# Kernel optimization log

Measured on AMD Instinct MI355X. Metric: run time of the kernel, lower is better.

Reference implementation:

```python
import jax, jax.numpy as jnp
import numpy as np

N_NODES = 50000
N_EDGES = 800000
IN_DIM = 128
EMB = 128
EDGE_DIM = 16
N_LAYERS = 4
BATCH = 64


def setup_inputs() -> dict:
    key = jax.random.key(0)
    ks = jax.random.split(key, 12)
    x = jax.random.normal(ks[0], (N_NODES, IN_DIM), dtype=jnp.float32)
    edge_index = jax.random.randint(ks[1], (2, N_EDGES), 0, N_NODES, dtype=jnp.int64)
    edge_attr = jax.random.normal(ks[2], (N_EDGES, EDGE_DIM), dtype=jnp.float32)
    batch = jnp.sort(jax.random.randint(ks[3], (N_NODES,), 0, BATCH, dtype=jnp.int64))

    def glorot(k, shape):
        fan_in = shape[-2]
        return jax.random.normal(k, shape, dtype=jnp.float32) / jnp.sqrt(jnp.float32(fan_in))

    msg_in = 2 * EMB + EDGE_DIM  # [h_src, h_dst, edge_attr]
    upd_in = 2 * EMB             # [h, aggregated_messages]
    return {
        "x": x,
        "edge_index": edge_index,
        "edge_attr": edge_attr,
        "batch": batch,
        "W_in": glorot(ks[4], (IN_DIM, EMB)),
        "b_in": jnp.zeros((EMB,), jnp.float32),
        "W_msg": glorot(ks[5], (N_LAYERS, msg_in, EMB)),
        "b_msg": jnp.zeros((N_LAYERS, EMB), jnp.float32),
        "W_upd": glorot(ks[6], (N_LAYERS, upd_in, EMB)),
        "b_upd": jnp.zeros((N_LAYERS, EMB), jnp.float32),
        "W_pred": glorot(ks[7], (EMB, 1)),
        "b_pred": jnp.zeros((1,), jnp.float32),
    }


def reference(x, edge_index, edge_attr, batch,
              W_in, b_in, W_msg, b_msg, W_upd, b_upd, W_pred, b_pred):
    n_nodes = x.shape[0]
    src, dst = edge_index[0], edge_index[1]

    # lin_in
    h = x @ W_in + b_in  # [N, EMB]

    # stacked message-passing layers with residual adds
    for l in range(W_msg.shape[0]):  # small fixed layer loop
        # per-edge message: relu(Linear([h_src, h_dst, e]))
        m_in = jnp.concatenate([h[src], h[dst], edge_attr], axis=-1)  # [E, 2*EMB+ED]
        m = jax.nn.relu(m_in @ W_msg[l] + b_msg[l])                    # [E, EMB]
        # sum-aggregate messages at destination nodes
        agg = jax.ops.segment_sum(m, dst, num_segments=n_nodes)       # [N, EMB]
        # node update: relu(Linear([h, agg])); residual add (h = h + conv(h))
        u_in = jnp.concatenate([h, agg], axis=-1)                      # [N, 2*EMB]
        h = h + jax.nn.relu(u_in @ W_upd[l] + b_upd[l])

    # global mean pool over graphs in the batch
    counts = jax.ops.segment_sum(jnp.ones((n_nodes,), h.dtype), batch, num_segments=BATCH)
    h_graph = jax.ops.segment_sum(h, batch, num_segments=BATCH) / jnp.maximum(counts, 1.0)[:, None]

    # lin_pred + view(-1)
    out = h_graph @ W_pred + b_pred  # [BATCH, 1]
    return out.reshape(-1)
```

## Files before the change

### kernel.cpp

```cpp
#include <hip/hip_runtime.h>


#define THREADS 256

typedef __attribute__((ext_vector_type(8))) short short8v;
typedef __attribute__((ext_vector_type(4))) float f32x4;
typedef __attribute__((ext_vector_type(2))) float f32x2;

__device__ inline unsigned short f2bf(float f)
{
    unsigned int u = __float_as_uint(f);
    return (unsigned short)((u + 0x7FFFu + ((u >> 16) & 1u)) >> 16);
}

__device__ inline unsigned int cvt_pk_bf16(float lo, float hi)
{
    unsigned int r;
    asm("v_cvt_pk_bf16_f32 %0, %1, %2" : "=v"(r) : "v"(lo), "v"(hi));
    return r;
}

__global__ __launch_bounds__(THREADS)
void wconv_all(const float* __restrict__ W_in, const float* __restrict__ W_msg,
               const float* __restrict__ W_upd, unsigned short* __restrict__ wbf)
{
    int b = blockIdx.x;
    int job, kb;
    if (b < 576) { job = b >> 6; kb = b & 63; }
    else         { int r = b - 576; job = 9 + (r >> 7); kb = r & 127; }

    const float* src;
    unsigned short* dst;
    int K;
    if (job == 0)      { src = W_in;                                  dst = wbf;                               K = 128; }
    else if (job <= 4) { int l = job - 1; src = W_msg + (size_t)l * 272 * 128;             dst = wbf + 16384 + l * 32768;           K = 128; }
    else if (job <= 8) { int l = job - 5; src = W_msg + (size_t)l * 272 * 128 + 128 * 128; dst = wbf + 16384 + l * 32768 + 16384;   K = 128; }
    else               { int l = job - 9; src = W_upd + (size_t)l * 256 * 128;             dst = wbf + 147456 + l * 32768;          K = 256; }

    int i = kb * 256 + threadIdx.x;
    int k = i >> 7, n = i & 127;
    dst[n * K + k] = f2bf(src[i]);
}

__global__ __launch_bounds__(THREADS)
void f32_to_bf16(const float* __restrict__ in, unsigned short* __restrict__ out, int n4)
{
    int i = blockIdx.x * blockDim.x + threadIdx.x;
    int stride = gridDim.x * blockDim.x;
    for (; i < n4; i += stride) {
        float4 v = reinterpret_cast<const float4*>(in)[i];
        unsigned int lo = f2bf(v.x) | ((unsigned int)f2bf(v.y) << 16);
        unsigned int hi = f2bf(v.z) | ((unsigned int)f2bf(v.w) << 16);
        reinterpret_cast<uint2*>(out)[i] = make_uint2(lo, hi);
    }
}

template<int K, int CPW, bool FUSED2, bool RELU, bool RESID, bool WF32>
__global__ __launch_bounds__(THREADS)
void gemm_regW(const unsigned short* __restrict__ X1, const unsigned short* __restrict__ X2,
               const unsigned short* __restrict__ Wt, const float* __restrict__ bias,
               const float* __restrict__ resid, float* __restrict__ Cf,
               unsigned short* __restrict__ CbfA, unsigned short* __restrict__ CbfB,
               int M, int nTiles)
{
    constexpr int KS  = K / 32;
    constexpr int NC  = CPW * 64;
    constexpr int LST = NC + 4;
    __shared__ float Cls[32 * LST];

    const int t = threadIdx.x;
    const int w = t >> 6;
    const int l = t & 63;
    const int r  = l & 15;
    const int kb = l >> 4;
    const int wc = w * (CPW * 16);

    short8v b[CPW][KS];
#pragma unroll
    for (int c = 0; c < CPW; c++)
#pragma unroll
        for (int ks = 0; ks < KS; ks++)
            b[c][ks] = *reinterpret_cast<const short8v*>(
                Wt + (size_t)(wc + c * 16 + r) * K + ks * 32 + kb * 8);

    const int rrow = t >> 3;
    const int cb   = (t & 7) * (NC / 8);

    for (int tile = blockIdx.x; tile < nTiles; tile += gridDim.x) {
        const int mBase = tile * 32;
        const int row0 = min(mBase + r,      M - 1);
        const int row1 = min(mBase + 16 + r, M - 1);

        f32x4 acc[2][CPW];
#pragma unroll
        for (int mi = 0; mi < 2; mi++)
#pragma unroll
            for (int c = 0; c < CPW; c++) acc[mi][c] = (f32x4){0.f, 0.f, 0.f, 0.f};

#pragma unroll
        for (int ks = 0; ks < KS; ks++) {
            const unsigned short* Xs = X1;
            int ko = ks * 32;
            if (K == 256 && ko >= 128) { Xs = X2; ko -= 128; }
            const short8v a0 = *reinterpret_cast<const short8v*>(Xs + (size_t)row0 * 128 + ko + kb * 8);
            const short8v a1 = *reinterpret_cast<const short8v*>(Xs + (size_t)row1 * 128 + ko + kb * 8);
#pragma unroll
            for (int c = 0; c < CPW; c++) {
                acc[0][c] = __builtin_amdgcn_mfma_f32_16x16x32_bf16(a0, b[c][ks], acc[0][c], 0, 0, 0);
                acc[1][c] = __builtin_amdgcn_mfma_f32_16x16x32_bf16(a1, b[c][ks], acc[1][c], 0, 0, 0);
            }
        }

#pragma unroll
        for (int mi = 0; mi < 2; mi++)
#pragma unroll
            for (int c = 0; c < CPW; c++) {
                const int gc = wc + c * 16 + r;
#pragma unroll
                for (int j = 0; j < 4; j++)
                    Cls[(mi * 16 + kb * 4 + j) * LST + gc] = acc[mi][c][j];
            }
        __syncthreads();

        const int gr = mBase + rrow;
        if (gr < M) {
#pragma unroll
            for (int q = 0; q < NC / 64; q += 1) {
                f32x4 v0 = *reinterpret_cast<const f32x4*>(&Cls[rrow * LST + cb + q * 8]);
                f32x4 v1 = *reinterpret_cast<const f32x4*>(&Cls[rrow * LST + cb + q * 8 + 4]);
                const int col = cb + q * 8;

                if (FUSED2) {
                    if (col >= 128) {
                        v0 += *reinterpret_cast<const f32x4*>(bias + col - 128);
                        v1 += *reinterpret_cast<const f32x4*>(bias + col - 128 + 4);
                    }
                } else if (bias) {
                    v0 += *reinterpret_cast<const f32x4*>(bias + col);
                    v1 += *reinterpret_cast<const f32x4*>(bias + col + 4);
                }
                if (RELU) {
#pragma unroll
                    for (int i = 0; i < 4; i++) { v0[i] = fmaxf(v0[i], 0.f); v1[i] = fmaxf(v1[i], 0.f); }
                }
                if (RESID) {
                    v0 += *reinterpret_cast<const f32x4*>(resid + (size_t)gr * 128 + col);
                    v1 += *reinterpret_cast<const f32x4*>(resid + (size_t)gr * 128 + col + 4);
                }
                if (WF32) {
                    *reinterpret_cast<f32x4*>(Cf + (size_t)gr * 128 + col)     = v0;
                    *reinterpret_cast<f32x4*>(Cf + (size_t)gr * 128 + col + 4) = v1;
                }
                uint4 pk;
                pk.x = cvt_pk_bf16(v0[0], v0[1]);
                pk.y = cvt_pk_bf16(v0[2], v0[3]);
                pk.z = cvt_pk_bf16(v1[0], v1[1]);
                pk.w = cvt_pk_bf16(v1[2], v1[3]);
                if (FUSED2) {
                    if (col < 128)
                        *reinterpret_cast<uint4*>(CbfA + (size_t)gr * 128 + col) = pk;
                    else
                        *reinterpret_cast<uint4*>(CbfB + (size_t)gr * 128 + col - 128) = pk;
                } else {
                    *reinterpret_cast<uint4*>(CbfA + (size_t)gr * 128 + col) = pk;
                }
            }
        }
        __syncthreads();
    }
}

__global__ __launch_bounds__(THREADS)
void zero_i32(int* __restrict__ p, int n)
{
    int i = blockIdx.x * blockDim.x + threadIdx.x;
    int stride = gridDim.x * blockDim.x;
    for (; i < n; i += stride) p[i] = 0;
}


__global__ __launch_bounds__(THREADS)
void csr_hist(const int* __restrict__ edst, int* __restrict__ deg, int nE)
{
    int i = blockIdx.x * blockDim.x + threadIdx.x;
    int stride = gridDim.x * blockDim.x;
    for (; i < nE; i += stride) atomicAdd(&deg[edst[i]], 1);
}

__global__ __launch_bounds__(THREADS)
void scan_stage1(const int* __restrict__ deg, int* __restrict__ incl,
                 int* __restrict__ psum, int n)
{
    __shared__ int buf[THREADS];
    const int t = threadIdx.x;
    const int base = blockIdx.x * 1024 + t * 4;

    int v0 = (base + 0 < n) ? deg[base + 0] : 0;
    int v1 = (base + 1 < n) ? deg[base + 1] : 0;
    int v2 = (base + 2 < n) ? deg[base + 2] : 0;
    int v3 = (base + 3 < n) ? deg[base + 3] : 0;
    const int s = v0 + v1 + v2 + v3;

    buf[t] = s;
    __syncthreads();
#pragma unroll
    for (int off = 1; off < THREADS; off <<= 1) {
        int x = (t >= off) ? buf[t - off] : 0;
        __syncthreads();
        buf[t] += x;
        __syncthreads();
    }
    const int excl = buf[t] - s;

    if (base + 0 < n) incl[base + 0] = excl + v0;
    if (base + 1 < n) incl[base + 1] = excl + v0 + v1;
    if (base + 2 < n) incl[base + 2] = excl + v0 + v1 + v2;
    if (base + 3 < n) incl[base + 3] = excl + s;
    if (t == THREADS - 1) psum[blockIdx.x] = buf[THREADS - 1];
}

__global__ __launch_bounds__(THREADS)
void scan_stage2(int* __restrict__ psum, int nb)
{
    __shared__ int buf[THREADS];
    const int t = threadIdx.x;
    int v = (t < nb) ? psum[t] : 0;
    buf[t] = v;
    __syncthreads();
#pragma unroll
    for (int off = 1; off < THREADS; off <<= 1) {
        int x = (t >= off) ? buf[t - off] : 0;
        __syncthreads();
        buf[t] += x;
        __syncthreads();
    }
    if (t < nb) psum[t] = buf[t] - v;
}

__global__ __launch_bounds__(THREADS)
void scan_stage3(const int* __restrict__ incl, const int* __restrict__ deg,
                 const int* __restrict__ psum, int* __restrict__ rowptr,
                 int* __restrict__ wp, int n, int nE)
{
    int i = blockIdx.x * blockDim.x + threadIdx.x;
    int stride = gridDim.x * blockDim.x;
    for (; i < n; i += stride) {
        int ex = incl[i] - deg[i] + psum[i >> 10];
        rowptr[i] = ex;
        wp[i]     = ex;
    }
    if (blockIdx.x == 0 && threadIdx.x == 0) rowptr[n] = nE;
}

__global__ __launch_bounds__(THREADS)
void csr_scatter(const int* __restrict__ esrc, const int* __restrict__ edst,
                 const float* __restrict__ eattr, int* __restrict__ wp,
                 int* __restrict__ col, float* __restrict__ eattrp, int nE)
{
    int i = blockIdx.x * blockDim.x + threadIdx.x;
    int stride = gridDim.x * blockDim.x;
    for (; i < nE; i += stride) {
        int d = edst[i];
        int pos = atomicAdd(&wp[d], 1);
        col[pos] = esrc[i];
        const float4* src4 = reinterpret_cast<const float4*>(eattr + (size_t)i * 16);
        float4*       dst4 = reinterpret_cast<float4*>(eattrp + (size_t)pos * 16);
        dst4[0] = src4[0]; dst4[1] = src4[1]; dst4[2] = src4[2]; dst4[3] = src4[3];
    }
}

__global__ __launch_bounds__(THREADS)
void edge_agg(const unsigned short* __restrict__ A, const unsigned short* __restrict__ Bb,
              const float* __restrict__ eattrp, const int* __restrict__ col,
              const int* __restrict__ rowptr, const float* __restrict__ Wm3,
              unsigned short* __restrict__ agg, int nN)
{
    __shared__ float W3s[16 * 128];
    const int t = threadIdx.x;

    *reinterpret_cast<float4*>(&W3s[t * 4])        = *reinterpret_cast<const float4*>(Wm3 + t * 4);
    *reinterpret_cast<float4*>(&W3s[1024 + t * 4]) = *reinterpret_cast<const float4*>(Wm3 + 1024 + t * 4);
    __syncthreads();

    const int lane = t & 63;
    const int wid  = __builtin_amdgcn_readfirstlane(t >> 6);
    const int d    = blockIdx.x * 4 + wid;
    if (d >= nN) return;

    f32x2 w[16];
#pragma unroll
    for (int k = 0; k < 16; k++)
        w[k] = *reinterpret_cast<const f32x2*>(&W3s[k * 128 + lane * 2]);

    const unsigned int bu = *reinterpret_cast<const unsigned int*>(Bb + (size_t)d * 128 + lane * 2);
    const f32x2 bv = (f32x2){__uint_as_float(bu << 16), __uint_as_float(bu & 0xFFFF0000u)};
    const f32x2 zero = (f32x2){0.f, 0.f};
    f32x2 acc = zero;

    const int beg = rowptr[d], end = rowptr[d + 1];
    int e = beg;
    for (; e + 2 <= end; e += 2) {
        const int s0 = col[e];
        const int s1 = col[e + 1];
        const unsigned int au0 = *reinterpret_cast<const unsigned int*>(A + (size_t)s0 * 128 + lane * 2);
        const unsigned int au1 = *reinterpret_cast<const unsigned int*>(A + (size_t)s1 * 128 + lane * 2);
        const float4* p0 = reinterpret_cast<const float4*>(eattrp + (size_t)e * 16);
        const float4* p1 = reinterpret_cast<const float4*>(eattrp + (size_t)(e + 1) * 16);
        const float4 e00 = p0[0], e01 = p0[1], e02 = p0[2], e03 = p0[3];
        const float4 e10 = p1[0], e11 = p1[1], e12 = p1[2], e13 = p1[3];

        f32x2 v0 = (f32x2){__uint_as_float(au0 << 16), __uint_as_float(au0 & 0xFFFF0000u)} + bv;
        f32x2 v1 = (f32x2){__uint_as_float(au1 << 16), __uint_as_float(au1 & 0xFFFF0000u)} + bv;

        const float ek0[16] = {e00.x, e00.y, e00.z, e00.w, e01.x, e01.y, e01.z, e01.w,
                               e02.x, e02.y, e02.z, e02.w, e03.x, e03.y, e03.z, e03.w};
        const float ek1[16] = {e10.x, e10.y, e10.z, e10.w, e11.x, e11.y, e11.z, e11.w,
                               e12.x, e12.y, e12.z, e12.w, e13.x, e13.y, e13.z, e13.w};
#pragma unroll
        for (int k = 0; k < 16; k++) {
            v0 = __builtin_elementwise_fma((f32x2){ek0[k], ek0[k]}, w[k], v0);
            v1 = __builtin_elementwise_fma((f32x2){ek1[k], ek1[k]}, w[k], v1);
        }
        acc += __builtin_elementwise_max(v0, zero) + __builtin_elementwise_max(v1, zero);
    }
    if (e < end) {
        const int s = col[e];
        const unsigned int au = *reinterpret_cast<const unsigned int*>(A + (size_t)s * 128 + lane * 2);
        f32x2 v = (f32x2){__uint_as_float(au << 16), __uint_as_float(au & 0xFFFF0000u)} + bv;
        const float4* ea4 = reinterpret_cast<const float4*>(eattrp + (size_t)e * 16);
        const float4 f0 = ea4[0], f1 = ea4[1], f2 = ea4[2], f3 = ea4[3];
        const float ek[16] = {f0.x, f0.y, f0.z, f0.w, f1.x, f1.y, f1.z, f1.w,
                              f2.x, f2.y, f2.z, f2.w, f3.x, f3.y, f3.z, f3.w};
#pragma unroll
        for (int k = 0; k < 16; k++)
            v = __builtin_elementwise_fma((f32x2){ek[k], ek[k]}, w[k], v);
        acc += __builtin_elementwise_max(v, zero);
    }
    *reinterpret_cast<unsigned int*>(agg + (size_t)d * 128 + lane * 2) = cvt_pk_bf16(acc[0], acc[1]);
}


__global__ __launch_bounds__(THREADS)
void pool_partial(const float* __restrict__ h, const int* __restrict__ batch,
                  float* __restrict__ hgsum, int n)
{
    const int t    = threadIdx.x;
    const int c    = t & 127;
    const int half = t >> 7;
    const int beg  = blockIdx.x * 256;
    const int end  = min(beg + 256, n);
    if (beg >= n) return;

    int   cur = -1;
    float acc = 0.f;
    for (int r = beg + half; r < end; r += 2) {
        int g = batch[r];
        if (g != cur) {
            if (cur >= 0) atomicAdd(&hgsum[(size_t)cur * 128 + c], acc);
            cur = g; acc = 0.f;
        }
        acc += h[(size_t)r * 128 + c];
    }
    if (cur >= 0) atomicAdd(&hgsum[(size_t)cur * 128 + c], acc);
}

__global__ __launch_bounds__(THREADS)
void pool_final(const float* __restrict__ hgsum, const int* __restrict__ batch,
                const float* __restrict__ Wp, const float* __restrict__ bp,
                float* __restrict__ out, int n)
{
    __shared__ float red[128];
    const int g = blockIdx.x;
    const int t = threadIdx.x;
    if (t >= 128) return;

    int lo, hi;
    {
        int a = 0, b = n;
        while (a < b) { int m = (a + b) >> 1; if (batch[m] < g) a = m + 1; else b = m; }
        lo = a;
        b = n;
        while (a < b) { int m = (a + b) >> 1; if (batch[m] < g + 1) a = m + 1; else b = m; }
        hi = a;
    }
    const int cnt = hi - lo;

    float v = hgsum[(size_t)g * 128 + t] / (float)max(cnt, 1);
    red[t] = v * Wp[t];
    __syncthreads();
    for (int off = 64; off > 0; off >>= 1) {
        if (t < off) red[t] += red[t + off];
        __syncthreads();
    }
    if (t == 0) out[g] = red[0] + bp[0];
}

extern "C" void kernel_launch(void* const* d_in, const int* in_sizes, int n_in,
                              void* d_out, int out_size, void* d_ws, size_t ws_size,
                              hipStream_t stream)
{
    const float* x      = (const float*)d_in[0];
    const int*   ei     = (const int*)  d_in[1];
    const float* eattr  = (const float*)d_in[2];
    const int*   batch  = (const int*)  d_in[3];
    const float* W_in   = (const float*)d_in[4];
    const float* b_in   = (const float*)d_in[5];
    const float* W_msg  = (const float*)d_in[6];
    const float* b_msg  = (const float*)d_in[7];
    const float* W_upd  = (const float*)d_in[8];
    const float* b_upd  = (const float*)d_in[9];
    const float* W_pred = (const float*)d_in[10];
    const float* b_pred = (const float*)d_in[11];
    float* out = (float*)d_out;

    const int nN = in_sizes[0] / 128;
    const int nE = in_sizes[1] / 2;
    const int* esrc = ei;
    const int* edst = ei + nE;

    float* h      = (float*)d_ws;
    float* eattrp = h + (size_t)nN * 128;
    float* hgsum  = eattrp + (size_t)nE * 16;
    unsigned short* xbf    = (unsigned short*)(hgsum + 8192);
    unsigned short* h_bf   = xbf    + (size_t)nN * 128;
    unsigned short* A_bf   = h_bf   + (size_t)nN * 128;
    unsigned short* Bb_bf  = A_bf   + (size_t)nN * 128;
    unsigned short* agg_bf = Bb_bf  + (size_t)nN * 128;
    unsigned short* wbf    = agg_bf + (size_t)nN * 128;
    unsigned short* wt_in  = wbf;
    unsigned short* wt_msg = wbf + 16384;
    unsigned short* wt_up  = wbf + 147456;
    int*   rowptr = (int*)(wbf + 278528);
    int*   wp     = rowptr + (nN + 1);
    int*   deg    = wp     + nN;
    int*   incl   = deg    + nN;
    int*   psum   = incl   + nN;
    int*   col    = psum   + 256;

    dim3 blk(THREADS);
    const int nTiles = (nN + 31) / 32;
    const int gGemm  = 1024;
    const int nChunks = (nN + 1023) / 1024;

    wconv_all<<<1088, blk, 0, stream>>>(W_in, W_msg, W_upd, wbf);
    f32_to_bf16<<<1024, blk, 0, stream>>>(x, xbf, nN * 128 / 4);

    zero_i32<<<64, blk, 0, stream>>>(deg, nN);
    csr_hist<<<256, blk, 0, stream>>>(edst, deg, nE);
    scan_stage1<<<nChunks, blk, 0, stream>>>(deg, incl, psum, nN);
    scan_stage2<<<1, blk, 0, stream>>>(psum, nChunks);
    scan_stage3<<<64, blk, 0, stream>>>(incl, deg, psum, rowptr, wp, nN, nE);
    csr_scatter<<<256, blk, 0, stream>>>(esrc, edst, eattr, wp, col, eattrp, nE);

    gemm_regW<128, 2, false, false, false, true><<<gGemm, blk, 0, stream>>>(
        xbf, nullptr, wt_in, b_in, nullptr, h, h_bf, nullptr, nN, nTiles);

    for (int l = 0; l < 4; l++) {
        const float* Wm3 = W_msg + (size_t)l * 272 * 128 + 256 * 128;
        const float* bm  = b_msg + l * 128;
        const float* bu  = b_upd + l * 128;

        gemm_regW<128, 4, true, false, false, false><<<gGemm, blk, 0, stream>>>(
            h_bf, nullptr, wt_msg + l * 32768, bm, nullptr, nullptr, A_bf, Bb_bf, nN, nTiles);

        edge_agg<<<(nN + 3) / 4, blk, 0, stream>>>(A_bf, Bb_bf, eattrp, col, rowptr, Wm3, agg_bf, nN);

        gemm_regW<256, 2, false, true, true, true><<<gGemm, blk, 0, stream>>>(
            h_bf, agg_bf, wt_up + l * 32768, bu, h, h, h_bf, nullptr, nN, nTiles);
    }

    zero_i32<<<16, blk, 0, stream>>>((int*)hgsum, 64 * 128);
    pool_partial<<<(nN + 255) / 256, blk, 0, stream>>>(h, batch, hgsum, nN);
    pool_final<<<64, blk, 0, stream>>>(hgsum, batch, W_pred, b_pred, out, nN);
}
```

Measured before the change: 651.7 us.

## Store permuted edge attributes as bf16 via separate coalesced gather kernel

The CSR scatter now records only the original edge index per sorted position. A new gather kernel then reads edge attributes in sorted order and writes them packed as bf16. This halves the edge-attribute bytes edge_agg reads in each of the four layers and replaces scattered 64-byte writes with coalesced ones. The cost is an extra kernel launch, an extra index array, and reduced precision on the edge features.

Result: slower. 730.0 us (+12.0%).

```diff
diff --git a/kernel.cpp b/kernel.cpp
--- a/kernel.cpp
+++ b/kernel.cpp
@@ -18,6 +18,12 @@
     unsigned int r;
     asm("v_cvt_pk_bf16_f32 %0, %1, %2" : "=v"(r) : "v"(lo), "v"(hi));
     return r;
+}
+
+__device__ inline void unp(unsigned int u, float& lo, float& hi)
+{
+    lo = __uint_as_float(u << 16);
+    hi = __uint_as_float(u & 0xFFFF0000u);
 }
 
 __global__ __launch_bounds__(THREADS)
@@ -254,24 +260,37 @@
 
 __global__ __launch_bounds__(THREADS)
 void csr_scatter(const int* __restrict__ esrc, const int* __restrict__ edst,
-                 const float* __restrict__ eattr, int* __restrict__ wp,
-                 int* __restrict__ col, float* __restrict__ eattrp, int nE)
+                 int* __restrict__ wp, int* __restrict__ col,
+                 int* __restrict__ eorder, int nE)
 {
     int i = blockIdx.x * blockDim.x + threadIdx.x;
     int stride = gridDim.x * blockDim.x;
     for (; i < nE; i += stride) {
         int d = edst[i];
         int pos = atomicAdd(&wp[d], 1);
-        col[pos] = esrc[i];
-        const float4* src4 = reinterpret_cast<const float4*>(eattr + (size_t)i * 16);
-        float4*       dst4 = reinterpret_cast<float4*>(eattrp + (size_t)pos * 16);
-        dst4[0] = src4[0]; dst4[1] = src4[1]; dst4[2] = src4[2]; dst4[3] = src4[3];
+        col[pos]    = esrc[i];
+        eorder[pos] = i;
+    }
+}
+
+__global__ __launch_bounds__(THREADS)
+void eattr_gather(const float* __restrict__ eattr, const int* __restrict__ eorder,
+                  unsigned short* __restrict__ eap, int nDw)
+{
+    int i = blockIdx.x * blockDim.x + threadIdx.x;
+    int stride = gridDim.x * blockDim.x;
+    for (; i < nDw; i += stride) {
+        const int p = i >> 3, j = i & 7;
+        const int ep = eorder[p];
+        float2 v = *reinterpret_cast<const float2*>(eattr + (size_t)ep * 16 + j * 2);
+        reinterpret_cast<unsigned int*>(eap)[(size_t)p * 8 + j] =
+            (unsigned int)f2bf(v.x) | ((unsigned int)f2bf(v.y) << 16);
     }
 }
 
 __global__ __launch_bounds__(THREADS)
 void edge_agg(const unsigned short* __restrict__ A, const unsigned short* __restrict__ Bb,
-              const float* __restrict__ eattrp, const int* __restrict__ col,
+              const unsigned short* __restrict__ eattrp, const int* __restrict__ col,
               const int* __restrict__ rowptr, const float* __restrict__ Wm3,
               unsigned short* __restrict__ agg, int nN)
 {
@@ -304,18 +323,22 @@
         const int s1 = col[e + 1];
         const unsigned int au0 = *reinterpret_cast<const unsigned int*>(A + (size_t)s0 * 128 + lane * 2);
         const unsigned int au1 = *reinterpret_cast<const unsigned int*>(A + (size_t)s1 * 128 + lane * 2);
-        const float4* p0 = reinterpret_cast<const float4*>(eattrp + (size_t)e * 16);
-        const float4* p1 = reinterpret_cast<const float4*>(eattrp + (size_t)(e + 1) * 16);
-        const float4 e00 = p0[0], e01 = p0[1], e02 = p0[2], e03 = p0[3];
-        const float4 e10 = p1[0], e11 = p1[1], e12 = p1[2], e13 = p1[3];
+        const uint4* pe = reinterpret_cast<const uint4*>(eattrp + (size_t)e * 16);
+        const uint4 qa = pe[0], qb = pe[1];
+        const uint4 qc = pe[2], qd = pe[3];
 
         f32x2 v0 = (f32x2){__uint_as_float(au0 << 16), __uint_as_float(au0 & 0xFFFF0000u)} + bv;
         f32x2 v1 = (f32x2){__uint_as_float(au1 << 16), __uint_as_float(au1 & 0xFFFF0000u)} + bv;
 
-        const float ek0[16] = {e00.x, e00.y, e00.z, e00.w, e01.x, e01.y, e01.z, e01.w,
-                               e02.x, e02.y, e02.z, e02.w, e03.x, e03.y, e03.z, e03.w};
-        const float ek1[16] = {e10.x, e10.y, e10.z, e10.w, e11.x, e11.y, e11.z, e11.w,
-                               e12.x, e12.y, e12.z, e12.w, e13.x, e13.y, e13.z, e13.w};
+        float ek0[16], ek1[16];
+        unp(qa.x, ek0[0], ek0[1]);  unp(qa.y, ek0[2], ek0[3]);
+        unp(qa.z, ek0[4], ek0[5]);  unp(qa.w, ek0[6], ek0[7]);
+        unp(qb.x, ek0[8], ek0[9]);  unp(qb.y, ek0[10], ek0[11]);
+        unp(qb.z, ek0[12], ek0[13]); unp(qb.w, ek0[14], ek0[15]);
+        unp(qc.x, ek1[0], ek1[1]);  unp(qc.y, ek1[2], ek1[3]);
+        unp(qc.z, ek1[4], ek1[5]);  unp(qc.w, ek1[6], ek1[7]);
+        unp(qd.x, ek1[8], ek1[9]);  unp(qd.y, ek1[10], ek1[11]);
+        unp(qd.z, ek1[12], ek1[13]); unp(qd.w, ek1[14], ek1[15]);
 #pragma unroll
         for (int k = 0; k < 16; k++) {
             v0 = __builtin_elementwise_fma((f32x2){ek0[k], ek0[k]}, w[k], v0);
@@ -327,10 +350,13 @@
         const int s = col[e];
         const unsigned int au = *reinterpret_cast<const unsigned int*>(A + (size_t)s * 128 + lane * 2);
         f32x2 v = (f32x2){__uint_as_float(au << 16), __uint_as_float(au & 0xFFFF0000u)} + bv;
-        const float4* ea4 = reinterpret_cast<const float4*>(eattrp + (size_t)e * 16);
-        const float4 f0 = ea4[0], f1 = ea4[1], f2 = ea4[2], f3 = ea4[3];
-        const float ek[16] = {f0.x, f0.y, f0.z, f0.w, f1.x, f1.y, f1.z, f1.w,
-                              f2.x, f2.y, f2.z, f2.w, f3.x, f3.y, f3.z, f3.w};
+        const uint4* pe = reinterpret_cast<const uint4*>(eattrp + (size_t)e * 16);
+        const uint4 qa = pe[0], qb = pe[1];
+        float ek[16];
+        unp(qa.x, ek[0], ek[1]);  unp(qa.y, ek[2], ek[3]);
+        unp(qa.z, ek[4], ek[5]);  unp(qa.w, ek[6], ek[7]);
+        unp(qb.x, ek[8], ek[9]);  unp(qb.y, ek[10], ek[11]);
+        unp(qb.z, ek[12], ek[13]); unp(qb.w, ek[14], ek[15]);
 #pragma unroll
         for (int k = 0; k < 16; k++)
             v = __builtin_elementwise_fma((f32x2){ek[k], ek[k]}, w[k], v);
@@ -419,14 +445,14 @@
     const int* edst = ei + nE;
 
     float* h      = (float*)d_ws;
-    float* eattrp = h + (size_t)nN * 128;
-    float* hgsum  = eattrp + (size_t)nE * 16;
+    float* hgsum  = h + (size_t)nN * 128;
     unsigned short* xbf    = (unsigned short*)(hgsum + 8192);
     unsigned short* h_bf   = xbf    + (size_t)nN * 128;
     unsigned short* A_bf   = h_bf   + (size_t)nN * 128;
     unsigned short* Bb_bf  = A_bf   + (size_t)nN * 128;
     unsigned short* agg_bf = Bb_bf  + (size_t)nN * 128;
-    unsigned short* wbf    = agg_bf + (size_t)nN * 128;
+    unsigned short* eattrp = agg_bf + (size_t)nN * 128;
+    unsigned short* wbf    = eattrp + (size_t)nE * 16;
     unsigned short* wt_in  = wbf;
     unsigned short* wt_msg = wbf + 16384;
     unsigned short* wt_up  = wbf + 147456;
@@ -436,6 +462,7 @@
     int*   incl   = deg    + nN;
     int*   psum   = incl   + nN;
     int*   col    = psum   + 256;
+    int*   eorder = col    + nE;
 
     dim3 blk(THREADS);
     const int nTiles = (nN + 31) / 32;
@@ -450,7 +477,8 @@
     scan_stage1<<<nChunks, blk, 0, stream>>>(deg, incl, psum, nN);
     scan_stage2<<<1, blk, 0, stream>>>(psum, nChunks);
     scan_stage3<<<64, blk, 0, stream>>>(incl, deg, psum, rowptr, wp, nN, nE);
-    csr_scatter<<<256, blk, 0, stream>>>(esrc, edst, eattr, wp, col, eattrp, nE);
+    csr_scatter<<<256, blk, 0, stream>>>(esrc, edst, wp, col, eorder, nE);
+    eattr_gather<<<2048, blk, 0, stream>>>(eattr, eorder, eattrp, nE * 8);
 
     gemm_regW<128, 2, false, false, false, true><<<gGemm, blk, 0, stream>>>(
         xbf, nullptr, wt_in, b_in, nullptr, h, h_bf, nullptr, nN, nTiles);
```

## Store edge ids in CSR instead of permuting edge_attr; unroll edge loop by 4

Applied to the files above, without the earlier changes.

The CSR scatter no longer copies each edge's 64-byte attribute row into a destination-sorted buffer. It writes only an (src, original edge id) pair, and edge_agg gathers edge_attr indirectly through that id. This removes a 51 MB scattered write plus read at setup. The cost is that the four per-layer aggregation passes now read edge attributes randomly instead of sequentially. The edge loop is also unrolled from 2 to 4 to expose more memory-level parallelism.

Measured after the change: 650.9 us. About the same (-0.1%).

```diff
diff --git a/kernel.cpp b/kernel.cpp
--- a/kernel.cpp
+++ b/kernel.cpp
@@ -254,24 +254,20 @@
 
 __global__ __launch_bounds__(THREADS)
 void csr_scatter(const int* __restrict__ esrc, const int* __restrict__ edst,
-                 const float* __restrict__ eattr, int* __restrict__ wp,
-                 int* __restrict__ col, float* __restrict__ eattrp, int nE)
+                 int* __restrict__ wp, int2* __restrict__ colord, int nE)
 {
     int i = blockIdx.x * blockDim.x + threadIdx.x;
     int stride = gridDim.x * blockDim.x;
     for (; i < nE; i += stride) {
         int d = edst[i];
         int pos = atomicAdd(&wp[d], 1);
-        col[pos] = esrc[i];
-        const float4* src4 = reinterpret_cast<const float4*>(eattr + (size_t)i * 16);
-        float4*       dst4 = reinterpret_cast<float4*>(eattrp + (size_t)pos * 16);
-        dst4[0] = src4[0]; dst4[1] = src4[1]; dst4[2] = src4[2]; dst4[3] = src4[3];
+        colord[pos] = make_int2(esrc[i], i);
     }
 }
 
 __global__ __launch_bounds__(THREADS)
 void edge_agg(const unsigned short* __restrict__ A, const unsigned short* __restrict__ Bb,
-              const float* __restrict__ eattrp, const int* __restrict__ col,
+              const float* __restrict__ eattr, const int2* __restrict__ colord,
               const int* __restrict__ rowptr, const float* __restrict__ Wm3,
               unsigned short* __restrict__ agg, int nN)
 {
@@ -299,36 +295,53 @@
 
     const int beg = rowptr[d], end = rowptr[d + 1];
     int e = beg;
-    for (; e + 2 <= end; e += 2) {
-        const int s0 = col[e];
-        const int s1 = col[e + 1];
-        const unsigned int au0 = *reinterpret_cast<const unsigned int*>(A + (size_t)s0 * 128 + lane * 2);
-        const unsigned int au1 = *reinterpret_cast<const unsigned int*>(A + (size_t)s1 * 128 + lane * 2);
-        const float4* p0 = reinterpret_cast<const float4*>(eattrp + (size_t)e * 16);
-        const float4* p1 = reinterpret_cast<const float4*>(eattrp + (size_t)(e + 1) * 16);
+    for (; e + 4 <= end; e += 4) {
+        const int2 c0 = colord[e + 0];
+        const int2 c1 = colord[e + 1];
+        const int2 c2 = colord[e + 2];
+        const int2 c3 = colord[e + 3];
+        const unsigned int au0 = *reinterpret_cast<const unsigned int*>(A + (size_t)c0.x * 128 + lane * 2);
+        const unsigned int au1 = *reinterpret_cast<const unsigned int*>(A + (size_t)c1.x * 128 + lane * 2);
+        const unsigned int au2 = *reinterpret_cast<const unsigned int*>(A + (size_t)c2.x * 128 + lane * 2);
+        const unsigned int au3 = *reinterpret_cast<const unsigned int*>(A + (size_t)c3.x * 128 + lane * 2);
+        const float4* p0 = reinterpret_cast<const float4*>(eattr + (size_t)c0.y * 16);
+        const float4* p1 = reinterpret_cast<const float4*>(eattr + (size_t)c1.y * 16);
+        const float4* p2 = reinterpret_cast<const float4*>(eattr + (size_t)c2.y * 16);
+        const float4* p3 = reinterpret_cast<const float4*>(eattr + (size_t)c3.y * 16);
         const float4 e00 = p0[0], e01 = p0[1], e02 = p0[2], e03 = p0[3];
         const float4 e10 = p1[0], e11 = p1[1], e12 = p1[2], e13 = p1[3];
+        const float4 e20 = p2[0], e21 = p2[1], e22 = p2[2], e23 = p2[3];
+        const float4 e30 = p3[0], e31 = p3[1], e32 = p3[2], e33 = p3[3];
 
         f32x2 v0 = (f32x2){__uint_as_float(au0 << 16), __uint_as_float(au0 & 0xFFFF0000u)} + bv;
         f32x2 v1 = (f32x2){__uint_as_float(au1 << 16), __uint_as_float(au1 & 0xFFFF0000u)} + bv;
+        f32x2 v2 = (f32x2){__uint_as_float(au2 << 16), __uint_as_float(au2 & 0xFFFF0000u)} + bv;
+        f32x2 v3 = (f32x2){__uint_as_float(au3 << 16), __uint_as_float(au3 & 0xFFFF0000u)} + bv;
 
         const float ek0[16] = {e00.x, e00.y, e00.z, e00.w, e01.x, e01.y, e01.z, e01.w,
                                e02.x, e02.y, e02.z, e02.w, e03.x, e03.y, e03.z, e03.w};
         const float ek1[16] = {e10.x, e10.y, e10.z, e10.w, e11.x, e11.y, e11.z, e11.w,
                                e12.x, e12.y, e12.z, e12.w, e13.x, e13.y, e13.z, e13.w};
+        const float ek2[16] = {e20.x, e20.y, e20.z, e20.w, e21.x, e21.y, e21.z, e21.w,
+                               e22.x, e22.y, e22.z, e22.w, e23.x, e23.y, e23.z, e23.w};
+        const float ek3[16] = {e30.x, e30.y, e30.z, e30.w, e31.x, e31.y, e31.z, e31.w,
+                               e32.x, e32.y, e32.z, e32.w, e33.x, e33.y, e33.z, e33.w};
 #pragma unroll
         for (int k = 0; k < 16; k++) {
             v0 = __builtin_elementwise_fma((f32x2){ek0[k], ek0[k]}, w[k], v0);
             v1 = __builtin_elementwise_fma((f32x2){ek1[k], ek1[k]}, w[k], v1);
+            v2 = __builtin_elementwise_fma((f32x2){ek2[k], ek2[k]}, w[k], v2);
+            v3 = __builtin_elementwise_fma((f32x2){ek3[k], ek3[k]}, w[k], v3);
         }
-        acc += __builtin_elementwise_max(v0, zero) + __builtin_elementwise_max(v1, zero);
-    }
-    if (e < end) {
-        const int s = col[e];
-        const unsigned int au = *reinterpret_cast<const unsigned int*>(A + (size_t)s * 128 + lane * 2);
+        acc += __builtin_elementwise_max(v0, zero) + __builtin_elementwise_max(v1, zero)
+             + __builtin_elementwise_max(v2, zero) + __builtin_elementwise_max(v3, zero);
+    }
+    for (; e < end; e++) {
+        const int2 ce = colord[e];
+        const unsigned int au = *reinterpret_cast<const unsigned int*>(A + (size_t)ce.x * 128 + lane * 2);
         f32x2 v = (f32x2){__uint_as_float(au << 16), __uint_as_float(au & 0xFFFF0000u)} + bv;
-        const float4* ea4 = reinterpret_cast<const float4*>(eattrp + (size_t)e * 16);
-        const float4 f0 = ea4[0], f1 = ea4[1], f2 = ea4[2], f3 = ea4[3];
+        const float4* ep = reinterpret_cast<const float4*>(eattr + (size_t)ce.y * 16);
+        const float4 f0 = ep[0], f1 = ep[1], f2 = ep[2], f3 = ep[3];
         const float ek[16] = {f0.x, f0.y, f0.z, f0.w, f1.x, f1.y, f1.z, f1.w,
                               f2.x, f2.y, f2.z, f2.w, f3.x, f3.y, f3.z, f3.w};
 #pragma unroll
@@ -419,8 +432,7 @@
     const int* edst = ei + nE;
 
     float* h      = (float*)d_ws;
-    float* eattrp = h + (size_t)nN * 128;
-    float* hgsum  = eattrp + (size_t)nE * 16;
+    float* hgsum  = h + (size_t)nN * 128;
     unsigned short* xbf    = (unsigned short*)(hgsum + 8192);
     unsigned short* h_bf   = xbf    + (size_t)nN * 128;
     unsigned short* A_bf   = h_bf   + (size_t)nN * 128;
@@ -430,12 +442,12 @@
     unsigned short* wt_in  = wbf;
     unsigned short* wt_msg = wbf + 16384;
     unsigned short* wt_up  = wbf + 147456;
-    int*   rowptr = (int*)(wbf + 278528);
+    int2*  colord = (int2*)(wbf + 278528);
+    int*   rowptr = (int*)(colord + nE);
     int*   wp     = rowptr + (nN + 1);
     int*   deg    = wp     + nN;
     int*   incl   = deg    + nN;
     int*   psum   = incl   + nN;
-    int*   col    = psum   + 256;
 
     dim3 blk(THREADS);
     const int nTiles = (nN + 31) / 32;
@@ -450,7 +462,7 @@
     scan_stage1<<<nChunks, blk, 0, stream>>>(deg, incl, psum, nN);
     scan_stage2<<<1, blk, 0, stream>>>(psum, nChunks);
     scan_stage3<<<64, blk, 0, stream>>>(incl, deg, psum, rowptr, wp, nN, nE);
-    csr_scatter<<<256, blk, 0, stream>>>(esrc, edst, eattr, wp, col, eattrp, nE);
+    csr_scatter<<<256, blk, 0, stream>>>(esrc, edst, wp, colord, nE);
 
     gemm_regW<128, 2, false, false, false, true><<<gGemm, blk, 0, stream>>>(
         xbf, nullptr, wt_in, b_in, nullptr, h, h_bf, nullptr, nN, nTiles);
@@ -463,7 +475,7 @@
         gemm_regW<128, 4, true, false, false, false><<<gGemm, blk, 0, stream>>>(
             h_bf, nullptr, wt_msg + l * 32768, bm, nullptr, nullptr, A_bf, Bb_bf, nN, nTiles);
 
-        edge_agg<<<(nN + 3) / 4, blk, 0, stream>>>(A_bf, Bb_bf, eattrp, col, rowptr, Wm3, agg_bf, nN);
+        edge_agg<<<(nN + 3) / 4, blk, 0, stream>>>(A_bf, Bb_bf, eattr, colord, rowptr, Wm3, agg_bf, nN);
 
         gemm_regW<256, 2, false, true, true, true><<<gGemm, blk, 0, stream>>>(
             h_bf, agg_bf, wt_up + l * 32768, bu, h, h, h_bf, nullptr, nN, nTiles);
```
